# Kernel optimization log

Hardware: AMD Instinct MI355X
Metric: run time of the kernel (lower is better)

## Reference

```python
import jax, jax.numpy as jnp
import numpy as np

B, S, HID = 2, 2048, 2048
NH, NKV, D = 16, 8, 128      # heads, kv heads, head_dim
G = NH // NKV                # kv groups = 2
THETA = 1000000.0


def setup_inputs() -> dict:
    key = jax.random.key(0)
    ks = jax.random.split(key, 8)
    std = 0.02
    return {
        "hidden_states": jax.random.normal(ks[0], (B, S, HID), dtype=jnp.float32),
        "Wq": jax.random.normal(ks[1], (HID, NH * D), dtype=jnp.float32) * std,
        "bq": jax.random.normal(ks[2], (NH * D,), dtype=jnp.float32) * std,
        "Wk": jax.random.normal(ks[3], (HID, NKV * D), dtype=jnp.float32) * std,
        "bk": jax.random.normal(ks[4], (NKV * D,), dtype=jnp.float32) * std,
        "Wv": jax.random.normal(ks[5], (HID, NKV * D), dtype=jnp.float32) * std,
        "bv": jax.random.normal(ks[6], (NKV * D,), dtype=jnp.float32) * std,
        "Wo": jax.random.normal(ks[7], (NH * D, HID), dtype=jnp.float32) * std,
    }


def _rope_tables(seq_len, dim, dtype):
    # freqs: [dim/2]; emb = cat([ang, ang], -1) as in the torch RotaryEmbedding
    freqs = 1.0 / (THETA ** (jnp.arange(0, dim, 2, dtype=jnp.float32) / dim))
    t = jnp.arange(seq_len, dtype=jnp.float32)
    ang = jnp.outer(t, freqs)                       # [S, D/2]
    emb = jnp.concatenate([ang, ang], axis=-1)      # [S, D]
    return jnp.cos(emb).astype(dtype), jnp.sin(emb).astype(dtype)


def _rotate_half(x):
    x1, x2 = x[..., : x.shape[-1] // 2], x[..., x.shape[-1] // 2:]
    return jnp.concatenate([-x2, x1], axis=-1)


def reference(hidden_states, Wq, bq, Wk, bk, Wv, bv, Wo):
    bs, s, _ = hidden_states.shape
    q = (hidden_states @ Wq + bq).reshape(bs, s, NH, D).transpose(0, 2, 1, 3)   # [B,NH,S,D]
    k = (hidden_states @ Wk + bk).reshape(bs, s, NKV, D).transpose(0, 2, 1, 3)  # [B,NKV,S,D]
    v = (hidden_states @ Wv + bv).reshape(bs, s, NKV, D).transpose(0, 2, 1, 3)

    cos, sin = _rope_tables(s, D, q.dtype)          # [S,D] each, broadcast over B,H
    q = q * cos + _rotate_half(q) * sin
    k = k * cos + _rotate_half(k) * sin

    # GQA without materializing repeated KV: group q heads by kv head
    qg = q.reshape(bs, NKV, G, s, D)
    scale = jnp.asarray(np.sqrt(D), q.dtype)
    scores = jnp.einsum('bkgsd,bktd->bkgst', qg, k) / scale  # [B,NKV,G,S,S]

    causal = jnp.tril(jnp.ones((s, s), dtype=bool))
    scores = jnp.where(causal, scores, jnp.asarray(-1e9, scores.dtype))

    probs = jax.nn.softmax(scores.astype(jnp.float32), axis=-1).astype(q.dtype)
    ctx = jnp.einsum('bkgst,bktd->bkgsd', probs, v)          # [B,NKV,G,S,D]
    ctx = ctx.reshape(bs, NH, s, D).transpose(0, 2, 1, 3).reshape(bs, s, NH * D)
    return ctx @ Wo
```

## Files before the change

kernel.cpp:

```cpp
#include <hip/hip_runtime.h>

typedef __bf16 bf16;
typedef __attribute__((ext_vector_type(8))) __bf16 bf16x8;
typedef __attribute__((ext_vector_type(4))) float f32x4;

constexpr int kS   = 2048;
constexpr int kNH  = 16;
constexpr int kNKV = 8;
constexpr int kD   = 128;
constexpr int kNqkv = 4096;

__device__ __forceinline__ void async_copy16(void* lds_base_uniform, const void* g) {
  __builtin_amdgcn_global_load_lds(
      (const __attribute__((address_space(1))) void*)g,
      (__attribute__((address_space(3))) void*)lds_base_uniform, 16, 0, 0);
}

__global__ void detect_dtype(const unsigned short* __restrict__ hs, int* __restrict__ flag) {
  __shared__ int cnt;
  if (threadIdx.x == 0) cnt = 0;
  __syncthreads();
  int local = 0;
  for (int i = threadIdx.x; i < 8192; i += 256) {
    int e = (hs[i] >> 7) & 0xFF;
    local += (e >= 0x85) ? 1 : 0;
  }
  atomicAdd(&cnt, local);
  __syncthreads();
  if (threadIdx.x == 0) flag[0] = (cnt > 256) ? 1 : 0;
}

__device__ __forceinline__ float ld_elem(const void* p, size_t i, int f32) {
  return f32 ? ((const float*)p)[i] : (float)((const bf16*)p)[i];
}

__device__ __forceinline__ bf16x8 load8(const void* base, size_t eoff, int f32) {
  if (f32) {
    const float* p = (const float*)base + eoff;
    f32x4 a = *(const f32x4*)p;
    f32x4 b = *(const f32x4*)(p + 4);
    bf16x8 r;
    r[0]=(bf16)a[0]; r[1]=(bf16)a[1]; r[2]=(bf16)a[2]; r[3]=(bf16)a[3];
    r[4]=(bf16)b[0]; r[5]=(bf16)b[1]; r[6]=(bf16)b[2]; r[7]=(bf16)b[3];
    return r;
  }
  return *(const bf16x8*)((const bf16*)base + eoff);
}

__global__ void convert_hs(const void* __restrict__ hs, bf16* __restrict__ out,
                           const int* __restrict__ flagp) {
  const int f32 = flagp[0];
  const size_t i = ((size_t)blockIdx.x * 256 + threadIdx.x) * 8;
  *(bf16x8*)(out + i) = load8(hs, i, f32);
}

__global__ void transpose_weights(const void* __restrict__ Wq, const void* __restrict__ Wk,
                                  const void* __restrict__ Wv, const void* __restrict__ Wo,
                                  bf16* __restrict__ WQKVT, bf16* __restrict__ WOT,
                                  const int* __restrict__ flagp, int zbase) {
  __shared__ bf16 tb[64][65];
  const int f32 = flagp[0];
  const int which = blockIdx.z + zbase;
  const void* src; bf16* dst; int N; int nbase;
  if      (which == 0) { src = Wq; dst = WQKVT; N = 2048; nbase = 0;    }
  else if (which == 1) { src = Wk; dst = WQKVT; N = 1024; nbase = 2048; }
  else if (which == 2) { src = Wv; dst = WQKVT; N = 1024; nbase = 3072; }
  else                 { src = Wo; dst = WOT;   N = 2048; nbase = 0;    }
  const int n0 = blockIdx.x * 64;
  if (n0 >= N) return;
  const int k0 = blockIdx.y * 64;
  const int tx = threadIdx.x & 63, ty = threadIdx.x >> 6;
#pragma unroll
  for (int i = 0; i < 16; ++i) {
    int ks = ty + 4*i;
    tb[ks][tx] = (bf16)ld_elem(src, (size_t)(k0 + ks) * N + n0 + tx, f32);
  }
  __syncthreads();
#pragma unroll
  for (int i = 0; i < 16; ++i) {
    int ns = ty + 4*i;
    dst[(size_t)(nbase + n0 + ns) * 2048 + k0 + tx] = tb[tx][ns];
  }
}

__global__ void concat_bias(const void* __restrict__ bq, const void* __restrict__ bk,
                            const void* __restrict__ bv, bf16* __restrict__ bias,
                            const int* __restrict__ flagp) {
  const int f32 = flagp[0];
  int i = blockIdx.x * 256 + threadIdx.x;
  float v;
  if (i < 2048)      v = ld_elem(bq, i, f32);
  else if (i < 3072) v = ld_elem(bk, i - 2048, f32);
  else               v = ld_elem(bv, i - 3072, f32);
  bias[i] = (bf16)v;
}

template<int BM>
__global__ __launch_bounds__(512, 2) void gemm_big_kernel(
    const bf16* __restrict__ A, const bf16* __restrict__ BT,
    const bf16* __restrict__ bias, void* __restrict__ C, int N, int K,
    const int* __restrict__ flagp, int c_ext, int mlog) {
  constexpr int RW = BM / 2;
  constexpr int AL = BM / 128;
  constexpr int ACN = RW / 16;
  constexpr int SLOT = BM * 64 + 16384;
  extern __shared__ bf16 lds[];
  const int cfl = c_ext ? flagp[0] : 0;
  const int t = threadIdx.x, lane = t & 63, wv = t >> 6;
  const int wm = wv >> 2, wn = wv & 3;
  const int quad = lane >> 4, l16 = lane & 15;

  const int f   = blockIdx.y * gridDim.x + blockIdx.x;
  const int tot = gridDim.x * gridDim.y;
  const int w   = (f & 7) * (tot >> 3) + (f >> 3);
  const int mb  = w & ((1 << mlog) - 1);
  const int nb  = w >> mlog;
  const int m0 = mb * BM, n0 = nb * 256;
  const int NT = K >> 6;

  const int soff = (l16 >> 1) * 64 + ((((l16 & 1) * 4 + quad) ^ (l16 >> 1)) * 8);

  f32x4 zero = {0.f, 0.f, 0.f, 0.f};
  f32x4 acc[ACN][4];
#pragma unroll
  for (int i = 0; i < ACN; ++i)
#pragma unroll
    for (int j = 0; j < 4; ++j) acc[i][j] = zero;

  auto vm_hold = [&]() {
    if constexpr (BM == 256) asm volatile("s_waitcnt vmcnt(4)" ::: "memory");
    else                     asm volatile("s_waitcnt vmcnt(3)" ::: "memory");
  };

  auto stageA = [&](int kt, int ks) {
    bf16* ub = lds + (size_t)(kt & 1) * SLOT + ks * (BM * 32);
#pragma unroll
    for (int q = 0; q < AL; ++q) {
      const int idx = q * 512 + t;
      const int line = idx >> 3;
      const int g = (idx & 7) ^ (line & 7);
      const int row = 2 * line + (g >> 2), ch = g & 3;
      async_copy16(ub + (size_t)(q * 512 + (t & ~63)) * 8,
                   A + (size_t)(m0 + row) * K + kt * 64 + ks * 32 + ch * 8);
    }
  };
  auto stageB = [&](int kt, int ks) {
    bf16* ub = lds + (size_t)(kt & 1) * SLOT + BM * 64 + ks * 8192;
#pragma unroll
    for (int q = 0; q < 2; ++q) {
      const int idx = q * 512 + t;
      const int line = idx >> 3;
      const int g = (idx & 7) ^ (line & 7);
      const int row = 2 * line + (g >> 2), ch = g & 3;
      async_copy16(ub + (size_t)(q * 512 + (t & ~63)) * 8,
                   BT + (size_t)(n0 + row) * K + kt * 64 + ks * 32 + ch * 8);
    }
  };

  stageA(0, 0); stageB(0, 0); stageA(0, 1); stageB(0, 1);
  vm_hold();
  __builtin_amdgcn_s_barrier();

  for (int jt = 0; jt < NT; ++jt) {
    const bf16* Abase = lds + (size_t)(jt & 1) * SLOT;
    const bf16* Bbase = Abase + BM * 64;
    const int nxt = (jt + 1 == NT) ? 0 : jt + 1;
#pragma unroll
    for (int ks = 0; ks < 2; ++ks) {
      const bf16* Au = Abase + ks * (BM * 32);
      const bf16* Bu = Bbase + ks * 8192;
      bf16x8 af[ACN], bfr[4];
#pragma unroll
      for (int mi = 0; mi < ACN; ++mi)
        af[mi] = *(const bf16x8*)(Au + (wm * RW + mi * 16) * 32 + soff);
#pragma unroll
      for (int ni = 0; ni < 4; ++ni)
        bfr[ni] = *(const bf16x8*)(Bu + (wn * 64 + ni * 16) * 32 + soff);

      stageA(nxt, ks); stageB(nxt, ks);

      __builtin_amdgcn_s_barrier();
      __builtin_amdgcn_s_setprio(1);
#pragma unroll
      for (int mi = 0; mi < ACN; ++mi)
#pragma unroll
        for (int ni = 0; ni < 4; ++ni)
          acc[mi][ni] = __builtin_amdgcn_mfma_f32_16x16x32_bf16(
              af[mi], bfr[ni], acc[mi][ni], 0, 0, 0);
      __builtin_amdgcn_s_setprio(0);
      vm_hold();
      __builtin_amdgcn_s_barrier();
    }
  }
  asm volatile("s_waitcnt vmcnt(0)" ::: "memory");

#pragma unroll
  for (int ni = 0; ni < 4; ++ni) {
    const int col = n0 + wn * 64 + ni * 16 + l16;
    const float bvf = bias ? (float)bias[col] : 0.0f;
#pragma unroll
    for (int mi = 0; mi < ACN; ++mi) {
      const int rowb = m0 + wm * RW + mi * 16 + quad * 4;
#pragma unroll
      for (int r = 0; r < 4; ++r) {
        const float v = acc[mi][ni][r] + bvf;
        const size_t idx = (size_t)(rowb + r) * N + col;
        if (cfl) ((float*)C)[idx] = v;
        else     ((bf16*)C)[idx]  = (bf16)v;
      }
    }
  }
}

__global__ void rope_kernel(bf16* __restrict__ C1) {
  const int tx = threadIdx.x & 63, ty = threadIdx.x >> 6;
  const int row = blockIdx.x * 4 + ty;
  const int hh = blockIdx.y;
  const int col = (hh < kNH) ? hh * kD : kNH*kD + (hh - kNH) * kD;
  const int s = row & (kS - 1);
  const float freq = __expf(-(float)tx * (13.815510557964274f / 64.0f));
  const float rev0 = (float)s * freq * 0.15915494309189535f;
  const float rev = rev0 - floorf(rev0);
  const float c  = __builtin_amdgcn_cosf(rev);
  const float sn = __builtin_amdgcn_sinf(rev);
  const size_t base = (size_t)row * kNqkv + col;
  const float x1 = (float)C1[base + tx];
  const float x2 = (float)C1[base + 64 + tx];
  C1[base + tx]      = (bf16)(x1 * c - x2 * sn);
  C1[base + 64 + tx] = (bf16)(x2 * c + x1 * sn);
}

__global__ void v_transpose(const bf16* __restrict__ C1, bf16* __restrict__ VT) {
  __shared__ bf16 tb[64][65];
  const int bkv = blockIdx.z;
  const int b = bkv >> 3, kv = bkv & 7;
  const int t0 = blockIdx.x * 64, d0 = blockIdx.y * 64;
  const int tx = threadIdx.x & 63, ty = threadIdx.x >> 6;
#pragma unroll
  for (int i = 0; i < 16; ++i) {
    int ts = ty + 4*i;
    tb[ts][tx] = C1[(size_t)(b*kS + t0 + ts) * kNqkv + 3072 + kv*kD + d0 + tx];
  }
  __syncthreads();
  const size_t obase = ((size_t)(b*kNKV + kv) * kD) * kS;
#pragma unroll
  for (int i = 0; i < 16; ++i) {
    int ds = ty + 4*i;
    VT[obase + (size_t)(d0 + ds) * kS + t0 + tx] = tb[tx][ds];
  }
}

__global__ __launch_bounds__(256) void attn_kernel(
    const bf16* __restrict__ C1, const bf16* __restrict__ VT, bf16* __restrict__ CTX) {
  constexpr int LDP = 72;
  __shared__ bf16 lds_k[2][64 * 128];
  __shared__ bf16 lds_v[2][128 * 64];
  __shared__ bf16 lds_p[4][16 * LDP];
  const int f = (blockIdx.z * gridDim.y + blockIdx.y) * gridDim.x + blockIdx.x;
  const int w = (f & 7) * 64 + (f >> 3);
  const int p = w & 15;
  const int rest = w >> 4;
  const int h = rest & 15;
  const int b = rest >> 4;
  const int qtA = 31 - p;
  const int qtB = p;
  const int kvh = h >> 1;
  const int t = threadIdx.x, lane = t & 63, wv = t >> 6;
  const int quad = lane >> 4, l16 = lane & 15;
  const float SC2 = 0.08838834764831845f * 1.4426950408889634f;

  bf16x8 qfA[4], qfB[4];
  {
    const size_t rowQA = (size_t)(b*kS + qtA*64 + wv*16 + l16) * kNqkv + h * kD;
    const size_t rowQB = (size_t)(b*kS + qtB*64 + wv*16 + l16) * kNqkv + h * kD;
#pragma unroll
    for (int c = 0; c < 4; ++c) {
      qfA[c] = *(const bf16x8*)(C1 + rowQA + c*32 + quad*8);
      qfB[c] = *(const bf16x8*)(C1 + rowQB + c*32 + quad*8);
    }
  }

  float lA[4] = {0,0,0,0}, lB[4] = {0,0,0,0};
  f32x4 oA[8], oB[8];
  f32x4 zero = {0.f, 0.f, 0.f, 0.f};
#pragma unroll
  for (int n = 0; n < 8; ++n) { oA[n] = zero; oB[n] = zero; }

  const int qrowA = qtA*64 + wv*16 + quad*4;
  const int qrowB = qtB*64 + wv*16 + quad*4;
  bf16* pw = &lds_p[wv][0];

  const size_t kbase = (size_t)b * kS * kNqkv + 2048 + kvh * kD;
  const size_t vbase = ((size_t)(b*kNKV + kvh) * kD) * kS;
  const int jv = (lane & 7) ^ ((lane >> 3) & 7);

  auto stage = [&](int buf, int k0) {
#pragma unroll
    for (int s2 = 0; s2 < 4; ++s2) {
      const int r = wv + s2 * 4;
      const int krow = r*4 + (lane >> 4);
      const int jk = (lane & 15) ^ (krow & 7);
      async_copy16(&lds_k[buf][r * 512], C1 + kbase + (size_t)(k0 + krow) * kNqkv + jk * 8);
      const int vrow = r*8 + (lane >> 3);
      async_copy16(&lds_v[buf][r * 512], VT + vbase + (size_t)vrow * kS + k0 + jv * 8);
    }
  };

  auto compute = [&](const bf16* kb_, const bf16* vb_, const bf16x8* qf,
                     f32x4* o_acc, float* l_acc, int qrow_base, int k0, bool diag) {
    f32x4 sc4[4];
    __builtin_amdgcn_s_setprio(1);
#pragma unroll
    for (int g = 0; g < 4; ++g) {
      f32x4 s_acc = zero;
#pragma unroll
      for (int c = 0; c < 4; ++c) {
        bf16x8 kf = *(const bf16x8*)(kb_ + (g*16 + l16) * 128 + (((c*4 + quad) ^ (l16 & 7)) * 8));
        s_acc = __builtin_amdgcn_mfma_f32_16x16x32_bf16(qf[c], kf, s_acc, 0, 0, 0);
      }
      sc4[g] = s_acc;
    }
    __builtin_amdgcn_s_setprio(0);
#pragma unroll
    for (int g = 0; g < 4; ++g) {
#pragma unroll
      for (int r = 0; r < 4; ++r) {
        float pv = __builtin_amdgcn_exp2f(fmaf(sc4[g][r], SC2, -24.f));
        if (diag && (k0 + g*16 + l16 > qrow_base + r)) pv = 0.f;
        l_acc[r] += pv;
        pw[(quad*4 + r) * LDP + g*16 + l16] = (bf16)pv;
      }
    }
    __builtin_amdgcn_wave_barrier();
    __builtin_amdgcn_s_setprio(1);
#pragma unroll
    for (int kk = 0; kk < 2; ++kk) {
      bf16x8 pf = *(const bf16x8*)(pw + l16 * LDP + kk*32 + quad*8);
#pragma unroll
      for (int n = 0; n < 8; ++n) {
        bf16x8 vf = *(const bf16x8*)(vb_ + (n*16 + l16) * 64 + (((kk*4 + quad) ^ (l16 & 7)) * 8));
        o_acc[n] = __builtin_amdgcn_mfma_f32_16x16x32_bf16(pf, vf, o_acc[n], 0, 0, 0);
      }
    }
    __builtin_amdgcn_s_setprio(0);
    __builtin_amdgcn_wave_barrier();
  };

  stage(0, 0);
  for (int kt = 0; kt <= qtA; ++kt) {
    const int cur = kt & 1;
    __syncthreads();
    if (kt + 1 <= qtA) stage(1 - cur, (kt + 1) * 64);
    const int k0 = kt * 64;
    compute(&lds_k[cur][0], &lds_v[cur][0], qfA, oA, lA, qrowA, k0, kt == qtA);
    if (kt <= qtB)
      compute(&lds_k[cur][0], &lds_v[cur][0], qfB, oB, lB, qrowB, k0, kt == qtB);
  }

  float invA[4], invB[4];
#pragma unroll
  for (int r = 0; r < 4; ++r) {
    float la = lA[r], lb = lB[r];
    la += __shfl_xor(la, 1); lb += __shfl_xor(lb, 1);
    la += __shfl_xor(la, 2); lb += __shfl_xor(lb, 2);
    la += __shfl_xor(la, 4); lb += __shfl_xor(lb, 4);
    la += __shfl_xor(la, 8); lb += __shfl_xor(lb, 8);
    invA[r] = 1.0f / la;     invB[r] = 1.0f / lb;
  }
#pragma unroll
  for (int n = 0; n < 8; ++n) {
#pragma unroll
    for (int r = 0; r < 4; ++r) {
      CTX[(size_t)(b*kS + qrowA + r) * (kNH*kD) + h*kD + n*16 + l16] = (bf16)(oA[n][r] * invA[r]);
      CTX[(size_t)(b*kS + qrowB + r) * (kNH*kD) + h*kD + n*16 + l16] = (bf16)(oB[n][r] * invB[r]);
    }
  }
}

extern "C" void kernel_launch(void* const* d_in, const int* in_sizes, int n_in,
                              void* d_out, int out_size, void* d_ws, size_t ws_size,
                              hipStream_t stream) {
  const void* hs = d_in[0];
  const void* Wq = d_in[1];
  const void* bq = d_in[2];
  const void* Wk = d_in[3];
  const void* bk = d_in[4];
  const void* Wv = d_in[5];
  const void* bv = d_in[6];
  const void* Wo = d_in[7];

  char* ws = (char*)d_ws;
  bf16* C1    = (bf16*)(ws + 0);
  bf16* WOT   = (bf16*)(ws + 0);
  bf16* WQKVT = (bf16*)(ws + 33554432);
  bf16* VT    = (bf16*)(ws + 33554432);
  bf16* CTX   = (bf16*)(ws + 41943040);
  bf16* HSB   = (bf16*)(ws + 58720256);
  bf16* BIAS  = (bf16*)(ws + 75497472);
  int*  FLAG  = (int*) (ws + 75505664);

  (void)hipFuncSetAttribute((const void*)gemm_big_kernel<256>,
                            hipFuncAttributeMaxDynamicSharedMemorySize, 131072);
  (void)hipFuncSetAttribute((const void*)gemm_big_kernel<128>,
                            hipFuncAttributeMaxDynamicSharedMemorySize, 98304);

  detect_dtype<<<1, 256, 0, stream>>>((const unsigned short*)hs, FLAG);
  convert_hs<<<4096, 256, 0, stream>>>(hs, HSB, FLAG);
  transpose_weights<<<dim3(32, 32, 3), 256, 0, stream>>>(Wq, Wk, Wv, Wo, WQKVT, WOT, FLAG, 0);
  concat_bias<<<16, 256, 0, stream>>>(bq, bk, bv, BIAS, FLAG);
  gemm_big_kernel<256><<<dim3(16, 16), 512, 131072, stream>>>(HSB, WQKVT, BIAS, C1, 4096, 2048, FLAG, 0, 4);
  rope_kernel<<<dim3(1024, 24), 256, 0, stream>>>(C1);
  v_transpose<<<dim3(32, 2, 16), 256, 0, stream>>>(C1, VT);
  attn_kernel<<<dim3(16, 16, 2), 256, 0, stream>>>(C1, VT, CTX);
  transpose_weights<<<dim3(32, 32, 1), 256, 0, stream>>>(Wq, Wk, Wv, Wo, WQKVT, WOT, FLAG, 3);
  gemm_big_kernel<128><<<dim3(8, 32), 512, 98304, stream>>>(CTX, WOT, nullptr, d_out, 2048, 2048, FLAG, 1, 5);
}
```

Measured before the change: 365.7 us.

## Replace async global-to-LDS copies with register-staged double-buffered GEMM pipeline

Swaps the direct global_load_lds async copies for global loads into registers that are later written to swizzled LDS, with two register sets giving a software pipeline one half-tile ahead. The k-loop is unrolled into two explicit half-steps that wait on lgkmcnt instead of vmcnt. Launch bounds drop to one block per SM so the extra staging registers fit. The cost is higher register pressure and lower occupancy, and the global-load latency now has to be hidden by the compute of one half-step.

```diff
diff --git a/kernel.cpp b/kernel.cpp
--- a/kernel.cpp
+++ b/kernel.cpp
@@ -96,7 +96,7 @@
 }
 
 template<int BM>
-__global__ __launch_bounds__(512, 2) void gemm_big_kernel(
+__global__ __launch_bounds__(512, 1) void gemm_big_kernel(
     const bf16* __restrict__ A, const bf16* __restrict__ BT,
     const bf16* __restrict__ bias, void* __restrict__ C, int N, int K,
     const int* __restrict__ flagp, int c_ext, int mlog) {
@@ -120,6 +120,8 @@
 
   const int soff = (l16 >> 1) * 64 + ((((l16 & 1) * 4 + quad) ^ (l16 >> 1)) * 8);
 
+  const int grow = t >> 2, gch = t & 3;
+
   f32x4 zero = {0.f, 0.f, 0.f, 0.f};
   f32x4 acc[ACN][4];
 #pragma unroll
@@ -127,58 +129,58 @@
 #pragma unroll
     for (int j = 0; j < 4; ++j) acc[i][j] = zero;
 
-  auto vm_hold = [&]() {
-    if constexpr (BM == 256) asm volatile("s_waitcnt vmcnt(4)" ::: "memory");
-    else                     asm volatile("s_waitcnt vmcnt(3)" ::: "memory");
+  f32x4 raX[AL], rbX[2], raY[AL], rbY[2];
+
+  auto gload = [&](int kt, int ks, f32x4* ra, f32x4* rb) {
+    const size_t ko = (size_t)kt * 64 + ks * 32 + gch * 8;
+#pragma unroll
+    for (int q = 0; q < AL; ++q)
+      ra[q] = *(const f32x4*)(A + (size_t)(m0 + q * 128 + grow) * K + ko);
+#pragma unroll
+    for (int q = 0; q < 2; ++q)
+      rb[q] = *(const f32x4*)(BT + (size_t)(n0 + q * 128 + grow) * K + ko);
   };
-
-  auto stageA = [&](int kt, int ks) {
-    bf16* ub = lds + (size_t)(kt & 1) * SLOT + ks * (BM * 32);
+  auto swrite = [&](int buf, int ks, const f32x4* ra, const f32x4* rb) {
+    bf16* Au = lds + (size_t)buf * SLOT + ks * (BM * 32);
+    bf16* Bu = lds + (size_t)buf * SLOT + BM * 64 + ks * 8192;
 #pragma unroll
     for (int q = 0; q < AL; ++q) {
-      const int idx = q * 512 + t;
-      const int line = idx >> 3;
-      const int g = (idx & 7) ^ (line & 7);
-      const int row = 2 * line + (g >> 2), ch = g & 3;
-      async_copy16(ub + (size_t)(q * 512 + (t & ~63)) * 8,
-                   A + (size_t)(m0 + row) * K + kt * 64 + ks * 32 + ch * 8);
+      const int r = q * 128 + grow, line = r >> 1;
+      const int s = ((r & 1) * 4 + gch) ^ (line & 7);
+      *(f32x4*)(Au + line * 64 + s * 8) = ra[q];
+    }
+#pragma unroll
+    for (int q = 0; q < 2; ++q) {
+      const int r = q * 128 + grow, line = r >> 1;
+      const int s = ((r & 1) * 4 + gch) ^ (line & 7);
+      *(f32x4*)(Bu + line * 64 + s * 8) = rb[q];
     }
   };
-  auto stageB = [&](int kt, int ks) {
-    bf16* ub = lds + (size_t)(kt & 1) * SLOT + BM * 64 + ks * 8192;
-#pragma unroll
-    for (int q = 0; q < 2; ++q) {
-      const int idx = q * 512 + t;
-      const int line = idx >> 3;
-      const int g = (idx & 7) ^ (line & 7);
-      const int row = 2 * line + (g >> 2), ch = g & 3;
-      async_copy16(ub + (size_t)(q * 512 + (t & ~63)) * 8,
-                   BT + (size_t)(n0 + row) * K + kt * 64 + ks * 32 + ch * 8);
-    }
-  };
-
-  stageA(0, 0); stageB(0, 0); stageA(0, 1); stageB(0, 1);
-  vm_hold();
+
+  gload(0, 0, raX, rbX); swrite(0, 0, raX, rbX);
+  gload(0, 1, raX, rbX); swrite(0, 1, raX, rbX);
+  gload((NT > 1) ? 1 : 0, 0, raY, rbY);
+  asm volatile("s_waitcnt lgkmcnt(0)" ::: "memory");
   __builtin_amdgcn_s_barrier();
 
   for (int jt = 0; jt < NT; ++jt) {
-    const bf16* Abase = lds + (size_t)(jt & 1) * SLOT;
+    const int cur = jt & 1;
+    const bf16* Abase = lds + (size_t)cur * SLOT;
     const bf16* Bbase = Abase + BM * 64;
-    const int nxt = (jt + 1 == NT) ? 0 : jt + 1;
-#pragma unroll
-    for (int ks = 0; ks < 2; ++ks) {
-      const bf16* Au = Abase + ks * (BM * 32);
-      const bf16* Bu = Bbase + ks * 8192;
+
+    {
       bf16x8 af[ACN], bfr[4];
 #pragma unroll
       for (int mi = 0; mi < ACN; ++mi)
-        af[mi] = *(const bf16x8*)(Au + (wm * RW + mi * 16) * 32 + soff);
+        af[mi] = *(const bf16x8*)(Abase + (wm * RW + mi * 16) * 32 + soff);
 #pragma unroll
       for (int ni = 0; ni < 4; ++ni)
-        bfr[ni] = *(const bf16x8*)(Bu + (wn * 64 + ni * 16) * 32 + soff);
-
-      stageA(nxt, ks); stageB(nxt, ks);
-
+        bfr[ni] = *(const bf16x8*)(Bbase + (wn * 64 + ni * 16) * 32 + soff);
+
+      gload((jt + 1 < NT) ? jt + 1 : 0, 1, raX, rbX);
+      swrite(1 - cur, 0, raY, rbY);
+
+      asm volatile("s_waitcnt lgkmcnt(0)" ::: "memory");
       __builtin_amdgcn_s_barrier();
       __builtin_amdgcn_s_setprio(1);
 #pragma unroll
@@ -188,11 +190,34 @@
           acc[mi][ni] = __builtin_amdgcn_mfma_f32_16x16x32_bf16(
               af[mi], bfr[ni], acc[mi][ni], 0, 0, 0);
       __builtin_amdgcn_s_setprio(0);
-      vm_hold();
+    }
+
+    {
+      const bf16* Au = Abase + BM * 32;
+      const bf16* Bu = Bbase + 8192;
+      bf16x8 af[ACN], bfr[4];
+#pragma unroll
+      for (int mi = 0; mi < ACN; ++mi)
+        af[mi] = *(const bf16x8*)(Au + (wm * RW + mi * 16) * 32 + soff);
+#pragma unroll
+      for (int ni = 0; ni < 4; ++ni)
+        bfr[ni] = *(const bf16x8*)(Bu + (wn * 64 + ni * 16) * 32 + soff);
+
+      gload((jt + 2 < NT) ? jt + 2 : 0, 0, raY, rbY);
+      swrite(1 - cur, 1, raX, rbX);
+
+      asm volatile("s_waitcnt lgkmcnt(0)" ::: "memory");
       __builtin_amdgcn_s_barrier();
-    }
-  }
-  asm volatile("s_waitcnt vmcnt(0)" ::: "memory");
+      __builtin_amdgcn_s_setprio(1);
+#pragma unroll
+      for (int mi = 0; mi < ACN; ++mi)
+#pragma unroll
+        for (int ni = 0; ni < 4; ++ni)
+          acc[mi][ni] = __builtin_amdgcn_mfma_f32_16x16x32_bf16(
+              af[mi], bfr[ni], acc[mi][ni], 0, 0, 0);
+      __builtin_amdgcn_s_setprio(0);
+    }
+  }
 
 #pragma unroll
   for (int ni = 0; ni < 4; ++ni) {
```

Result: no change. 369.4 us (+1.0%).
